# Performance work log

Hardware: AMD Instinct MI355X
Metric: run time of the kernel (lower is better)

## Reference

```python
import jax, jax.numpy as jnp
import numpy as np

N_NODES = 100000
N_EDGES = 300000
D_IN = 256
D_OUT = 256


def setup_inputs() -> dict:
    key = jax.random.key(0)
    k1, k2, k3 = jax.random.split(key, 3)
    z = jax.random.normal(k1, (N_NODES, D_IN), dtype=jnp.float32)
    edge_index = jax.random.randint(k2, (2, N_EDGES), 0, N_NODES, dtype=jnp.int64)
    # Linear(input_dim, out_dim): weight [out, in], stored transposed for x @ W
    W = jax.random.normal(k3, (D_IN, D_OUT), dtype=jnp.float32) / np.sqrt(D_IN)
    b = jnp.zeros((D_OUT,), dtype=jnp.float32)
    return {"z": z, "edge_index": edge_index, "W": W, "b": b}


def reference(z, edge_index, W, b):
    # h = Linear(z): [N, D_out]
    h = z @ W + b
    # gather endpoint embeddings and take per-edge dot product
    src = h[edge_index[0]]  # [E, D_out]
    dst = h[edge_index[1]]  # [E, D_out]
    value = jnp.sum(src * dst, axis=1)  # [E]
    return jax.nn.sigmoid(value)
```

## Files before the change

### kernel.cpp

```cpp
#include <hip/hip_runtime.h>
#include <hip/hip_bf16.h>
#include <hip/hip_fp16.h>
#include <math.h>


#define D_DIM 256
#define BM 128

typedef __attribute__((ext_vector_type(8))) short bf16x8;
typedef __attribute__((ext_vector_type(4))) float f32x4;

__device__ bf16x8 g_Wh[8 * 256 * 4];
__device__ bf16x8 g_Wl[8 * 256 * 4];

__device__ inline unsigned short bf16_rn(float x) {
  unsigned u = __builtin_bit_cast(unsigned, x);
  unsigned r = u + 0x7FFFu + ((u >> 16) & 1u);
  return (unsigned short)(r >> 16);
}
__device__ inline float bf16_f(unsigned short s) {
  return __builtin_bit_cast(float, (unsigned)s << 16);
}

__device__ inline void split8(const float4 f0, const float4 f1, bf16x8& hi, bf16x8& lo) {
  float v[8] = {f0.x, f0.y, f0.z, f0.w, f1.x, f1.y, f1.z, f1.w};
#pragma unroll
  for (int j = 0; j < 8; j++) {
    unsigned short hb = bf16_rn(v[j]);
    hi[j] = (short)hb;
    lo[j] = (short)bf16_rn(v[j] - bf16_f(hb));
  }
}

__global__ __launch_bounds__(256) void pack_w_kernel(const float* __restrict__ W) {
  int t = blockIdx.x * 256 + threadIdx.x;
  int kb = t >> 10;
  int qd = (t >> 8) & 3;
  int n  = t & 255;
  float v[8];
#pragma unroll
  for (int j = 0; j < 8; j++)
    v[j] = W[(size_t)(kb * 32 + qd * 8 + j) * D_DIM + n];
  bf16x8 hi, lo;
  split8(make_float4(v[0], v[1], v[2], v[3]),
         make_float4(v[4], v[5], v[6], v[7]), hi, lo);
  int fi = (kb * 256 + n) * 4 + qd;
  g_Wh[fi] = hi;
  g_Wl[fi] = lo;
}

__device__ inline void stage_b(int kb, char* buf, int wv, int lane) {
  const char* gsrc = (wv < 4)
      ? ((const char*)g_Wh + (size_t)kb * 16384 + (wv & 3) * 4096)
      : ((const char*)g_Wl + (size_t)kb * 16384 + (wv & 3) * 4096);
  char* ldst = buf + ((wv < 4) ? 0 : 16384) + (wv & 3) * 4096;
#pragma unroll
  for (int i = 0; i < 4; i++) {
    __builtin_amdgcn_global_load_lds(
        (const __attribute__((address_space(1))) void*)(gsrc + i * 1024 + lane * 16),
        (__attribute__((address_space(3))) void*)(ldst + i * 1024),
        16, 0, 0);
  }
}

__global__ __launch_bounds__(512) void gemm_mfma_kernel(
    const float* __restrict__ z, const float* __restrict__ b,
    __half* __restrict__ h, int nrows) {
  __shared__ char smem[2 * 32768];
  const int tid = threadIdx.x;
  const int lane = tid & 63;
  const int wv = tid >> 6;
  const int mg = wv >> 1;
  const int nh = wv & 1;
  const int fr = lane & 15;
  const int qd = lane >> 4;
  const int row0 = blockIdx.x * BM + mg * 32;

  f32x4 acc[2][8];
#pragma unroll
  for (int i = 0; i < 2; i++)
#pragma unroll
    for (int j = 0; j < 8; j++) acc[i][j] = (f32x4)0.f;

  const float* zp[2];
#pragma unroll
  for (int fm = 0; fm < 2; fm++) {
    int r = row0 + fm * 16 + fr;
    r = r < nrows ? r : (nrows - 1);
    zp[fm] = z + (size_t)r * D_DIM + qd * 8;
  }

  float4 a0[2], a1[2];
#pragma unroll
  for (int fm = 0; fm < 2; fm++) {
    a0[fm] = *(const float4*)(zp[fm]);
    a1[fm] = *(const float4*)(zp[fm] + 4);
  }
  stage_b(0, smem, wv, lane);
  __syncthreads();

#pragma unroll 2
  for (int kb = 0; kb < 8; kb++) {
    char* cur = smem + (kb & 1) * 32768;
    if (kb < 7) stage_b(kb + 1, smem + ((kb + 1) & 1) * 32768, wv, lane);

    bf16x8 ah[2], al[2];
#pragma unroll
    for (int fm = 0; fm < 2; fm++) split8(a0[fm], a1[fm], ah[fm], al[fm]);
    if (kb < 7) {
#pragma unroll
      for (int fm = 0; fm < 2; fm++) {
        const float* p = zp[fm] + (kb + 1) * 32;
        a0[fm] = *(const float4*)(p);
        a1[fm] = *(const float4*)(p + 4);
      }
    }

    const bf16x8* bufh = (const bf16x8*)cur;
    const bf16x8* bufl = (const bf16x8*)(cur + 16384);
#pragma unroll
    for (int fn = 0; fn < 8; fn++) {
      int fi = (nh * 128 + fn * 16 + fr) * 4 + qd;
      bf16x8 bh = bufh[fi];
      bf16x8 bl = bufl[fi];
#pragma unroll
      for (int fm = 0; fm < 2; fm++) {
        acc[fm][fn] = __builtin_amdgcn_mfma_f32_16x16x32_bf16(ah[fm], bh, acc[fm][fn], 0, 0, 0);
        acc[fm][fn] = __builtin_amdgcn_mfma_f32_16x16x32_bf16(ah[fm], bl, acc[fm][fn], 0, 0, 0);
        acc[fm][fn] = __builtin_amdgcn_mfma_f32_16x16x32_bf16(al[fm], bh, acc[fm][fn], 0, 0, 0);
      }
    }
    __syncthreads();
  }

  __half* et = (__half*)(smem + wv * 4608);
  float bias[8];
#pragma unroll
  for (int fn = 0; fn < 8; fn++) bias[fn] = b[nh * 128 + fn * 16 + fr];

#pragma unroll
  for (int fm = 0; fm < 2; fm++) {
#pragma unroll
    for (int fn = 0; fn < 8; fn++)
#pragma unroll
      for (int r = 0; r < 4; r++)
        et[(qd * 4 + r) * 136 + fn * 16 + fr] = __float2half(acc[fm][fn][r] + bias[fn]);
#pragma unroll
    for (int p = 0; p < 4; p++) {
      int idx = p * 64 + lane;
      int rr = idx >> 4;
      int cc = idx & 15;
      float4 v = *(const float4*)(et + rr * 136 + cc * 8);
      int row = row0 + fm * 16 + rr;
      if (row < nrows)
        *(float4*)(h + (size_t)row * D_DIM + nh * 128 + cc * 8) = v;
    }
  }
}

__global__ __launch_bounds__(256) void edge_dot_kernel(
    const int* __restrict__ ei, const __half* __restrict__ h,
    float* __restrict__ out, int E) {
  int wid = (blockIdx.x * blockDim.x + threadIdx.x) >> 6;
  int lane = threadIdx.x & 63;
  int ebase = wid * 8;
  if (ebase >= E) return;
  const int half = lane >> 5;
  const int off = lane & 31;

  float4 v[8];
#pragma unroll
  for (int q = 0; q < 8; q++) {
    int e = ebase + q;
    e = e < E ? e : (E - 1);
    int node = half ? ei[E + e] : ei[e];
    v[q] = *(const float4*)((const __half*)h + (size_t)node * D_DIM + off * 8);
  }

  float res = 0.f;
#pragma unroll
  for (int q = 0; q < 8; q++) {
    float4 w;
    w.x = __shfl_xor(v[q].x, 32);
    w.y = __shfl_xor(v[q].y, 32);
    w.z = __shfl_xor(v[q].z, 32);
    w.w = __shfl_xor(v[q].w, 32);
    const __half2* a2 = (const __half2*)&v[q];
    const __half2* b2 = (const __half2*)&w;
    float part = 0.f;
#pragma unroll
    for (int j = 0; j < 4; j++) {
      float2 fa = __half22float2(a2[j]);
      float2 fb = __half22float2(b2[j]);
      part += fa.x * fb.x + fa.y * fb.y;
    }
#pragma unroll
    for (int m = 1; m <= 16; m <<= 1) part += __shfl_xor(part, m);
    res = (lane == q) ? part : res;
  }
  if (lane < 8) {
    int e = ebase + lane;
    if (e < E) out[e] = 1.0f / (1.0f + __expf(-res));
  }
}

extern "C" void kernel_launch(void* const* d_in, const int* in_sizes, int n_in,
                              void* d_out, int out_size, void* d_ws, size_t ws_size,
                              hipStream_t stream) {
  const float* z  = (const float*)d_in[0];
  const int*   ei = (const int*)d_in[1];
  const float* W  = (const float*)d_in[2];
  const float* b  = (const float*)d_in[3];
  float* out = (float*)d_out;
  __half* h  = (__half*)d_ws;

  const int nnodes = in_sizes[0] / D_DIM;
  const int E = in_sizes[1] / 2;

  pack_w_kernel<<<32, 256, 0, stream>>>(W);

  dim3 grid_gemm((nnodes + BM - 1) / BM);
  gemm_mfma_kernel<<<grid_gemm, 512, 0, stream>>>(z, b, h, nnodes);

  int waves = (E + 7) / 8;
  dim3 grid_edge(((size_t)waves * 64 + 255) / 256);
  edge_dot_kernel<<<grid_edge, 256, 0, stream>>>(ei, h, out, E);
}
```

Before: 246.1 us.

## Shrink GEMM tile to 64 rows, single-buffer LDS, truncating bf16 split

Halves the GEMM row tile so each wave computes one 16-row fragment instead of two, and drops the double-buffered B staging in favour of a single 32KB LDS buffer guarded by two barriers per k-step. It also swaps the round-to-nearest hi/lo bf16 split of z for a cheaper truncation split. The aim is to cut registers and LDS per block so more blocks fit per CU, with cheaper per-element conversion. In exchange, B is reloaded from global/L2 twice as often per row, the overlap of B staging with MFMA is lost, and truncating the split costs some precision.

```diff
diff --git a/kernel.cpp b/kernel.cpp
--- a/kernel.cpp
+++ b/kernel.cpp
@@ -5,7 +5,7 @@
 
 
 #define D_DIM 256
-#define BM 128
+#define BM 64
 
 typedef __attribute__((ext_vector_type(8))) short bf16x8;
 typedef __attribute__((ext_vector_type(4))) float f32x4;
@@ -22,13 +22,32 @@
   return __builtin_bit_cast(float, (unsigned)s << 16);
 }
 
-__device__ inline void split8(const float4 f0, const float4 f1, bf16x8& hi, bf16x8& lo) {
+__device__ inline void split8_rne(const float4 f0, const float4 f1, bf16x8& hi, bf16x8& lo) {
   float v[8] = {f0.x, f0.y, f0.z, f0.w, f1.x, f1.y, f1.z, f1.w};
 #pragma unroll
   for (int j = 0; j < 8; j++) {
     unsigned short hb = bf16_rn(v[j]);
     hi[j] = (short)hb;
     lo[j] = (short)bf16_rn(v[j] - bf16_f(hb));
+  }
+}
+
+__device__ inline void split8_trunc(const float4 f0, const float4 f1, bf16x8& hi, bf16x8& lo) {
+  unsigned u[8];
+  u[0] = __builtin_bit_cast(unsigned, f0.x); u[1] = __builtin_bit_cast(unsigned, f0.y);
+  u[2] = __builtin_bit_cast(unsigned, f0.z); u[3] = __builtin_bit_cast(unsigned, f0.w);
+  u[4] = __builtin_bit_cast(unsigned, f1.x); u[5] = __builtin_bit_cast(unsigned, f1.y);
+  u[6] = __builtin_bit_cast(unsigned, f1.z); u[7] = __builtin_bit_cast(unsigned, f1.w);
+  unsigned* hp = (unsigned*)&hi;
+  unsigned* lp = (unsigned*)&lo;
+#pragma unroll
+  for (int p = 0; p < 4; p++) {
+    unsigned a = u[2 * p], c = u[2 * p + 1];
+    hp[p] = (a >> 16) | (c & 0xFFFF0000u);
+    float la = __builtin_bit_cast(float, a) - __builtin_bit_cast(float, a & 0xFFFF0000u);
+    float lc = __builtin_bit_cast(float, c) - __builtin_bit_cast(float, c & 0xFFFF0000u);
+    lp[p] = (__builtin_bit_cast(unsigned, la) >> 16) |
+            (__builtin_bit_cast(unsigned, lc) & 0xFFFF0000u);
   }
 }
 
@@ -42,8 +61,8 @@
   for (int j = 0; j < 8; j++)
     v[j] = W[(size_t)(kb * 32 + qd * 8 + j) * D_DIM + n];
   bf16x8 hi, lo;
-  split8(make_float4(v[0], v[1], v[2], v[3]),
-         make_float4(v[4], v[5], v[6], v[7]), hi, lo);
+  split8_rne(make_float4(v[0], v[1], v[2], v[3]),
+             make_float4(v[4], v[5], v[6], v[7]), hi, lo);
   int fi = (kb * 256 + n) * 4 + qd;
   g_Wh[fi] = hi;
   g_Wl[fi] = lo;
@@ -66,95 +85,72 @@
 __global__ __launch_bounds__(512) void gemm_mfma_kernel(
     const float* __restrict__ z, const float* __restrict__ b,
     __half* __restrict__ h, int nrows) {
-  __shared__ char smem[2 * 32768];
+  __shared__ char smem[34816];
   const int tid = threadIdx.x;
   const int lane = tid & 63;
   const int wv = tid >> 6;
-  const int mg = wv >> 1;
+  const int mf = wv >> 1;
   const int nh = wv & 1;
   const int fr = lane & 15;
   const int qd = lane >> 4;
-  const int row0 = blockIdx.x * BM + mg * 32;
-
-  f32x4 acc[2][8];
-#pragma unroll
-  for (int i = 0; i < 2; i++)
-#pragma unroll
-    for (int j = 0; j < 8; j++) acc[i][j] = (f32x4)0.f;
-
-  const float* zp[2];
-#pragma unroll
-  for (int fm = 0; fm < 2; fm++) {
-    int r = row0 + fm * 16 + fr;
-    r = r < nrows ? r : (nrows - 1);
-    zp[fm] = z + (size_t)r * D_DIM + qd * 8;
-  }
-
-  float4 a0[2], a1[2];
-#pragma unroll
-  for (int fm = 0; fm < 2; fm++) {
-    a0[fm] = *(const float4*)(zp[fm]);
-    a1[fm] = *(const float4*)(zp[fm] + 4);
-  }
-  stage_b(0, smem, wv, lane);
-  __syncthreads();
-
-#pragma unroll 2
+  const int row0 = blockIdx.x * BM + mf * 16;
+
+  f32x4 acc[8];
+#pragma unroll
+  for (int j = 0; j < 8; j++) acc[j] = (f32x4)0.f;
+
+  int ar = row0 + fr;
+  ar = ar < nrows ? ar : (nrows - 1);
+  const float* zrow = z + (size_t)ar * D_DIM + qd * 8;
+
+  float4 a0 = *(const float4*)(zrow);
+  float4 a1 = *(const float4*)(zrow + 4);
+
+#pragma unroll 1
   for (int kb = 0; kb < 8; kb++) {
-    char* cur = smem + (kb & 1) * 32768;
-    if (kb < 7) stage_b(kb + 1, smem + ((kb + 1) & 1) * 32768, wv, lane);
-
-    bf16x8 ah[2], al[2];
-#pragma unroll
-    for (int fm = 0; fm < 2; fm++) split8(a0[fm], a1[fm], ah[fm], al[fm]);
+    __syncthreads();
+    stage_b(kb, smem, wv, lane);
+    bf16x8 ah, al;
+    split8_trunc(a0, a1, ah, al);
+    __syncthreads();
     if (kb < 7) {
-#pragma unroll
-      for (int fm = 0; fm < 2; fm++) {
-        const float* p = zp[fm] + (kb + 1) * 32;
-        a0[fm] = *(const float4*)(p);
-        a1[fm] = *(const float4*)(p + 4);
-      }
+      const float* p = zrow + (kb + 1) * 32;
+      a0 = *(const float4*)(p);
+      a1 = *(const float4*)(p + 4);
     }
-
-    const bf16x8* bufh = (const bf16x8*)cur;
-    const bf16x8* bufl = (const bf16x8*)(cur + 16384);
+    const bf16x8* bufh = (const bf16x8*)smem;
+    const bf16x8* bufl = (const bf16x8*)(smem + 16384);
 #pragma unroll
     for (int fn = 0; fn < 8; fn++) {
       int fi = (nh * 128 + fn * 16 + fr) * 4 + qd;
       bf16x8 bh = bufh[fi];
       bf16x8 bl = bufl[fi];
-#pragma unroll
-      for (int fm = 0; fm < 2; fm++) {
-        acc[fm][fn] = __builtin_amdgcn_mfma_f32_16x16x32_bf16(ah[fm], bh, acc[fm][fn], 0, 0, 0);
-        acc[fm][fn] = __builtin_amdgcn_mfma_f32_16x16x32_bf16(ah[fm], bl, acc[fm][fn], 0, 0, 0);
-        acc[fm][fn] = __builtin_amdgcn_mfma_f32_16x16x32_bf16(al[fm], bh, acc[fm][fn], 0, 0, 0);
-      }
+      acc[fn] = __builtin_amdgcn_mfma_f32_16x16x32_bf16(ah, bh, acc[fn], 0, 0, 0);
+      acc[fn] = __builtin_amdgcn_mfma_f32_16x16x32_bf16(ah, bl, acc[fn], 0, 0, 0);
+      acc[fn] = __builtin_amdgcn_mfma_f32_16x16x32_bf16(al, bh, acc[fn], 0, 0, 0);
     }
-    __syncthreads();
-  }
-
-  __half* et = (__half*)(smem + wv * 4608);
+  }
+  __syncthreads();
+
+  __half* et = (__half*)(smem + wv * 4352);
   float bias[8];
 #pragma unroll
   for (int fn = 0; fn < 8; fn++) bias[fn] = b[nh * 128 + fn * 16 + fr];
 
 #pragma unroll
-  for (int fm = 0; fm < 2; fm++) {
-#pragma unroll
-    for (int fn = 0; fn < 8; fn++)
-#pragma unroll
-      for (int r = 0; r < 4; r++)
-        et[(qd * 4 + r) * 136 + fn * 16 + fr] = __float2half(acc[fm][fn][r] + bias[fn]);
-#pragma unroll
-    for (int p = 0; p < 4; p++) {
-      int idx = p * 64 + lane;
-      int rr = idx >> 4;
-      int cc = idx & 15;
-      float4 v = *(const float4*)(et + rr * 136 + cc * 8);
-      int row = row0 + fm * 16 + rr;
-      if (row < nrows)
-        *(float4*)(h + (size_t)row * D_DIM + nh * 128 + cc * 8) = v;
-    }
+  for (int fn = 0; fn < 8; fn++)
+#pragma unroll
+    for (int r = 0; r < 4; r++)
+      et[(qd * 4 + r) * 136 + fn * 16 + fr] = __float2half(acc[fn][r] + bias[fn]);
+#pragma unroll
+  for (int p = 0; p < 4; p++) {
+    int idx = p * 64 + lane;
+    int rr = idx >> 4;
+    int cc = idx & 15;
+    float4 v = *(const float4*)(et + rr * 136 + cc * 8);
+    int row = row0 + rr;
+    if (row < nrows)
+      *(float4*)(h + (size_t)row * D_DIM + nh * 128 + cc * 8) = v;
   }
 }
 
```

Result: faster. 230.7 us (-6.2%).
